# Performance work log

Measured on AMD Instinct MI355X. Metric: run time of the kernel, lower is better.

The kernel has to match this reference:

```python
import jax, jax.numpy as jnp
import numpy as np
from jax import lax

SL, BS, D, H, T = 256, 64, 1024, 512, 17
BN_EPS = 1e-5


def setup_inputs() -> dict:
    key = jax.random.key(0)
    ks = jax.random.split(key, 16)
    k = 1.0 / np.sqrt(H)
    u = lambda kk, shape: jax.random.uniform(kk, shape, jnp.float32, -k, k)
    word_input = jax.random.normal(ks[0], (SL, BS, D), jnp.float32)
    lengths = jax.random.randint(ks[1], (BS,), SL // 2, SL + 1)
    mask = jnp.arange(SL)[:, None] < lengths[None, :]  # (SL, BS), first step all valid
    labels = jax.random.randint(ks[2], (SL, BS), 0, T)
    return dict(
        word_input=word_input, mask=mask, labels=labels,
        w_ih_f=u(ks[3], (4 * H, D)), w_hh_f=u(ks[4], (4 * H, H)),
        b_ih_f=u(ks[5], (4 * H,)), b_hh_f=u(ks[6], (4 * H,)),
        w_ih_b=u(ks[7], (4 * H, D)), w_hh_b=u(ks[8], (4 * H, H)),
        b_ih_b=u(ks[9], (4 * H,)), b_hh_b=u(ks[10], (4 * H,)),
        bn_gamma=jnp.ones((2 * H,), jnp.float32), bn_beta=jnp.zeros((2 * H,), jnp.float32),
        lin_w=u(ks[11], (T, 2 * H)), lin_b=u(ks[12], (T,)),
        crf_start=0.1 * jax.random.normal(ks[13], (T,), jnp.float32),
        crf_end=0.1 * jax.random.normal(ks[14], (T,), jnp.float32),
        crf_trans=0.1 * jax.random.normal(ks[15], (T, T), jnp.float32),
    )


def _lstm_dir(x, w_ih, w_hh, b_ih, b_hh, reverse):
    # x: (SL, BS, D); PyTorch gate order i, f, g, o
    B = x.shape[1]
    h0 = jnp.zeros((B, H), x.dtype)
    xg = jnp.einsum('sbd,gd->sbg', x, w_ih) + b_ih + b_hh  # precompute input projections

    def step(carry, xt):
        h, c = carry
        g = xt + h @ w_hh.T
        i, f, gg, o = jnp.split(g, 4, axis=-1)
        c = jax.nn.sigmoid(f) * c + jax.nn.sigmoid(i) * jnp.tanh(gg)
        h = jax.nn.sigmoid(o) * jnp.tanh(c)
        return (h, c), h

    _, hs = lax.scan(step, (h0, h0), xg, reverse=reverse)
    return hs  # (SL, BS, H)


def _crf_llh(E, y, m, start, end, trans):
    # E: (B, L, T) batch-first emissions; y: (B, L) int; m: (B, L) bool
    B = E.shape[0]
    mf = m.astype(E.dtype)
    b = jnp.arange(B)
    # numerator (gold path score)
    emit = jnp.take_along_axis(E, y[:, :, None], axis=2)[:, :, 0]  # (B, L)
    num = start[y[:, 0]] + emit[:, 0]
    tr = trans[y[:, :-1], y[:, 1:]]  # (B, L-1)
    num = num + jnp.sum(mf[:, 1:] * (tr + emit[:, 1:]), axis=1)
    last = jnp.sum(m.astype(jnp.int32), axis=1) - 1
    num = num + end[y[b, last]]
    # partition function via forward algorithm
    alpha0 = start + E[:, 0]  # (B, T)

    def step(alpha, inp):
        e_t, m_t = inp
        nxt = jax.nn.logsumexp(alpha[:, :, None] + trans[None], axis=1) + e_t
        return jnp.where(m_t[:, None], nxt, alpha), None

    alpha, _ = lax.scan(step, alpha0, (E[:, 1:].transpose(1, 0, 2), m[:, 1:].T))
    Z = jax.nn.logsumexp(alpha + end, axis=1)
    return jnp.sum(num - Z)


def _viterbi(E, m, start, end, trans):
    # E: (B, L, T); m: (B, L) bool -> padded tags (B, L)
    B = E.shape[0]
    b = jnp.arange(B)
    score0 = start + E[:, 0]  # (B, T)

    def fwd(score, inp):
        e_t, m_t = inp
        cand = score[:, :, None] + trans[None]  # (B, T, T)
        best_prev = jnp.argmax(cand, axis=1)  # (B, T)
        best = jnp.max(cand, axis=1) + e_t
        return jnp.where(m_t[:, None], best, score), best_prev

    final, history = lax.scan(fwd, score0, (E[:, 1:].transpose(1, 0, 2), m[:, 1:].T))
    last_tag = jnp.argmax(final + end, axis=1)  # (B,)

    def bwd(tag, inp):
        bp, m_t = inp
        prev = jnp.where(m_t, bp[b, tag], tag)
        return prev, tag

    tag0, tags_rest = lax.scan(bwd, last_tag, (history, m[:, 1:].T), reverse=True)
    tags = jnp.concatenate([tag0[None], tags_rest], axis=0).T  # (B, L)
    return jnp.where(m, tags, 0)


def _forward(word_input, mask, labels, w_ih_f, w_hh_f, b_ih_f, b_hh_f,
             w_ih_b, w_hh_b, b_ih_b, b_hh_b, bn_gamma, bn_beta, lin_w, lin_b,
             crf_start, crf_end, crf_trans):
    hf = _lstm_dir(word_input, w_ih_f, w_hh_f, b_ih_f, b_hh_f, reverse=False)
    hb = _lstm_dir(word_input, w_ih_b, w_hh_b, b_ih_b, b_hh_b, reverse=True)
    lstm_out = jnp.concatenate([hf, hb], axis=-1)  # (SL, BS, 2H)
    x = lstm_out.reshape(-1, 2 * H)
    mean = x.mean(0)
    var = x.var(0)  # biased, as in torch BN training normalization
    xn = (x - mean) / jnp.sqrt(var + BN_EPS) * bn_gamma + bn_beta
    logits = xn @ lin_w.T + lin_b  # (SL*BS, T)
    E = logits.reshape(SL, BS, T).transpose(1, 0, 2)  # batch-first (B, L, T)
    m = mask.T  # (B, L)
    loss = -_crf_llh(E, labels.T, m, crf_start, crf_end, crf_trans)
    preds = _viterbi(E, m, crf_start, crf_end, crf_trans)
    return loss, preds


def reference(word_input, mask, labels, w_ih_f, w_hh_f, b_ih_f, b_hh_f,
              w_ih_b, w_hh_b, b_ih_b, b_hh_b, bn_gamma, bn_beta, lin_w, lin_b,
              crf_start, crf_end, crf_trans):
    return _forward(word_input, mask, labels, w_ih_f, w_hh_f, b_ih_f, b_hh_f,
                    w_ih_b, w_hh_b, b_ih_b, b_hh_b, bn_gamma, bn_beta, lin_w, lin_b,
                    crf_start, crf_end, crf_trans)
```

## Files before the change

### kernel.cpp

```cpp
#include <hip/hip_runtime.h>
#include <hip/hip_bf16.h>
#include <math.h>

#define SL 256
#define BS 64
#define DI 1024
#define HH 512
#define TT 17
#define NR (SL*BS)
#define G4 (4*HH)
#define C2 (2*HH)
#define NBLK 128

__device__ __forceinline__ float sigm(float x) { return 1.f / (1.f + expf(-x)); }

typedef float vfloat4 __attribute__((ext_vector_type(4)));

__device__ __forceinline__ void coh_load4(float4& d, const float* p) {
    asm volatile("global_load_dwordx4 %0, %1, off sc0 sc1" : "=v"(d) : "v"(p) : "memory");
}
__device__ __forceinline__ void coh_load4i(int4& d, const int* p) {
    asm volatile("global_load_dwordx4 %0, %1, off sc0 sc1" : "=v"(d) : "v"(p) : "memory");
}
__device__ __forceinline__ void coh_store4(const float4& d, float* p) {
    vfloat4 t; t.x = d.x; t.y = d.y; t.z = d.z; t.w = d.w;
    asm volatile("global_store_dwordx4 %0, %1, off sc0 sc1" :: "v"(p), "v"(t) : "memory");
}
__device__ __forceinline__ void wait_vm0() { asm volatile("s_waitcnt vmcnt(0)" ::: "memory"); }

__global__ __launch_bounds__(256) void pack_whh_v3(const float* __restrict__ whh,
                                                   float* __restrict__ wp)
{
    const int s = blockIdx.x;
    for (int idx = threadIdx.x; idx < 512 * 24; idx += 256) {
        const int k = idx / 24, c = idx % 24;
        float v = 0.f;
        if (c < 16) {
            const int g = c >> 2, uu = c & 3;
            v = whh[(size_t)(g * 512 + 4 * s + uu) * HH + k];
        }
        wp[(size_t)s * 12288 + idx] = v;
    }
}

__global__ __launch_bounds__(512) void init_flags(int* __restrict__ f)
{
    f[blockIdx.x * 512 + threadIdx.x] = 0;
}

__global__ __launch_bounds__(256) void gemm_xg(
    const float* __restrict__ A,
    const float* __restrict__ W,
    const float* __restrict__ b1,
    const float* __restrict__ b2,
    float* __restrict__ C)
{
    __shared__ float As[16][128];
    __shared__ float Bs[16][128];
    const int tid = threadIdx.x;
    const int m0 = blockIdx.x * 128;
    const int n0 = blockIdx.y * 128;
    const int tm = tid >> 4;
    const int tn = tid & 15;
    const int lr = tid >> 2;
    const int lc = (tid & 3) * 4;

    float acc[8][8];
    #pragma unroll
    for (int i = 0; i < 8; i++)
        #pragma unroll
        for (int j = 0; j < 8; j++) acc[i][j] = 0.f;

    for (int kt = 0; kt < DI; kt += 16) {
        #pragma unroll
        for (int p = 0; p < 2; p++) {
            float4 v = *(const float4*)(A + (size_t)(m0 + p * 64 + lr) * DI + kt + lc);
            As[lc + 0][p * 64 + lr] = v.x;
            As[lc + 1][p * 64 + lr] = v.y;
            As[lc + 2][p * 64 + lr] = v.z;
            As[lc + 3][p * 64 + lr] = v.w;
            float4 w = *(const float4*)(W + (size_t)(n0 + p * 64 + lr) * DI + kt + lc);
            Bs[lc + 0][p * 64 + lr] = w.x;
            Bs[lc + 1][p * 64 + lr] = w.y;
            Bs[lc + 2][p * 64 + lr] = w.z;
            Bs[lc + 3][p * 64 + lr] = w.w;
        }
        __syncthreads();
        #pragma unroll
        for (int kk = 0; kk < 16; kk++) {
            float4 a0 = *(const float4*)&As[kk][tm * 8];
            float4 a1 = *(const float4*)&As[kk][tm * 8 + 4];
            float4 bv0 = *(const float4*)&Bs[kk][tn * 8];
            float4 bv1 = *(const float4*)&Bs[kk][tn * 8 + 4];
            float a[8] = {a0.x, a0.y, a0.z, a0.w, a1.x, a1.y, a1.z, a1.w};
            float b[8] = {bv0.x, bv0.y, bv0.z, bv0.w, bv1.x, bv1.y, bv1.z, bv1.w};
            #pragma unroll
            for (int i = 0; i < 8; i++)
                #pragma unroll
                for (int j = 0; j < 8; j++)
                    acc[i][j] = fmaf(a[i], b[j], acc[i][j]);
        }
        __syncthreads();
    }
    const int g  = n0 >> 9;
    const int u0 = (n0 & 511) + tn * 8;
    const int s0 = u0 >> 2;
    #pragma unroll
    for (int i = 0; i < 8; i++) {
        const int m = m0 + tm * 8 + i;
        const int mt = m >> 6, mb = m & 63;
        #pragma unroll
        for (int sj = 0; sj < 4; sj++) {
            const int n = n0 + tn * 8 + sj * 2;
            float2 v;
            v.x = acc[i][sj * 2 + 0] + b1[n + 0] + b2[n + 0];
            v.y = acc[i][sj * 2 + 1] + b1[n + 1] + b2[n + 1];
            *(float2*)(C + ((((size_t)(s0 + (sj >> 1)) * SL + mt) * BS + mb) << 4)
                         + g * 4 + 2 * (sj & 1)) = v;
        }
    }
}

__global__ __launch_bounds__(512, 2) void lstm_flag(
    const float* __restrict__ xg_f, const float* __restrict__ xg_b,
    const float* __restrict__ wp_f, const float* __restrict__ wp_b,
    float* __restrict__ Hf, float* __restrict__ Hb,
    int* __restrict__ flag_f, int* __restrict__ flag_b,
    float* __restrict__ out,
    int dir_base)
{
    __shared__ float w_s[512 * 24];
    __shared__ float hs[128 * 68];
    __shared__ float g_s[16 * 65];
    __shared__ float hpub[256];
    float* const part = hs;

    const int dir = dir_base + (blockIdx.x >> 7);
    const int s   = blockIdx.x & 127;
    const float* xg  = dir ? xg_b : xg_f;
    const float* wp  = dir ? wp_b : wp_f;
    float* Hbuf      = dir ? Hb : Hf;
    int*   flag      = dir ? flag_b : flag_f;
    const int reverse = dir;
    const int col_off = dir * HH;

    const int tid = threadIdx.x;
    const int ks  = tid >> 4;
    const int bt  = (tid >> 1) & 7;
    const int ct  = tid & 1;
    const int wv  = tid >> 6;

    {
        const float4* src = (const float4*)(wp + (size_t)s * 12288);
        float4* dst = (float4*)w_s;
        for (int i = tid; i < 3072; i += 512) dst[i] = src[i];
    }

    const float* xgs = xg + (size_t)s * (SL * 1024);
    float cst = 0.f;
    float4 r[4];
    float4 acc[8][2];

    for (int step = 0; step < SL; ++step) {
        const int t = reverse ? (SL - 1 - step) : step;
        const float myxg0 = xgs[t * 1024 + tid];
        const float myxg1 = xgs[t * 1024 + 512 + tid];

        if (step > 0) {
            if (tid < 32) {
                const int* fp = flag + (step - 1) * NBLK + tid * 4;
                int4 f;
                for (;;) {
                    coh_load4i(f, fp);
                    wait_vm0();
                    if (f.x & f.y & f.z & f.w) break;
                    __builtin_amdgcn_s_sleep(1);
                }
            }
            __syncthreads();

            const float* hsrc = Hbuf + ((step + 1) & 1) * (512 * 64);
            #pragma unroll
            for (int i = 0; i < 4; ++i)
                coh_load4(r[i], hsrc + (size_t)(i * 512 + tid) * 4);

            #pragma unroll
            for (int i = 0; i < 8; ++i) {
                acc[i][0] = make_float4(0.f, 0.f, 0.f, 0.f);
                acc[i][1] = make_float4(0.f, 0.f, 0.f, 0.f);
            }

            for (int kc = 0; kc < 4; ++kc) {
                if (kc) __syncthreads();
                wait_vm0();
                #pragma unroll
                for (int i = 0; i < 4; ++i) {
                    const int idx = i * 512 + tid;
                    const int k = idx >> 4, b4 = (idx & 15) * 4;
                    *(float4*)&hs[k * 68 + b4] = r[i];
                }
                __syncthreads();
                if (kc < 3) {
                    const float* base = hsrc + (size_t)(kc + 1) * 8192;
                    #pragma unroll
                    for (int i = 0; i < 4; ++i)
                        coh_load4(r[i], base + (size_t)(i * 512 + tid) * 4);
                }
                #pragma unroll
                for (int j = 0; j < 4; ++j) {
                    const int kk = ks + 32 * j;
                    const int kg = kc * 128 + kk;
                    const float4 w0 = *(const float4*)&w_s[kg * 24 + ct * 8];
                    const float4 w1 = *(const float4*)&w_s[kg * 24 + ct * 8 + 4];
                    const float* hp = &hs[kk * 68 + 8 * bt];
                    const float2 h01 = *(const float2*)(hp + 0);
                    const float2 h23 = *(const float2*)(hp + 2);
                    const float2 h45 = *(const float2*)(hp + 4);
                    const float2 h67 = *(const float2*)(hp + 6);
                    const float hv[8] = {h01.x, h01.y, h23.x, h23.y, h45.x, h45.y, h67.x, h67.y};
                    #pragma unroll
                    for (int i = 0; i < 8; ++i) {
                        acc[i][0].x = fmaf(hv[i], w0.x, acc[i][0].x);
                        acc[i][0].y = fmaf(hv[i], w0.y, acc[i][0].y);
                        acc[i][0].z = fmaf(hv[i], w0.z, acc[i][0].z);
                        acc[i][0].w = fmaf(hv[i], w0.w, acc[i][0].w);
                        acc[i][1].x = fmaf(hv[i], w1.x, acc[i][1].x);
                        acc[i][1].y = fmaf(hv[i], w1.y, acc[i][1].y);
                        acc[i][1].z = fmaf(hv[i], w1.z, acc[i][1].z);
                        acc[i][1].w = fmaf(hv[i], w1.w, acc[i][1].w);
                    }
                }
            }
            #pragma unroll
            for (int i = 0; i < 8; ++i)
                #pragma unroll
                for (int p = 0; p < 2; ++p) {
                    acc[i][p].x += __shfl_xor(acc[i][p].x, 16);
                    acc[i][p].y += __shfl_xor(acc[i][p].y, 16);
                    acc[i][p].z += __shfl_xor(acc[i][p].z, 16);
                    acc[i][p].w += __shfl_xor(acc[i][p].w, 16);
                    acc[i][p].x += __shfl_xor(acc[i][p].x, 32);
                    acc[i][p].y += __shfl_xor(acc[i][p].y, 32);
                    acc[i][p].z += __shfl_xor(acc[i][p].z, 32);
                    acc[i][p].w += __shfl_xor(acc[i][p].w, 32);
                }
            __syncthreads();
            if ((tid & 63) < 16) {
                #pragma unroll
                for (int i = 0; i < 8; ++i) {
                    const int base = wv * 1088 + (8 * bt + i) * 16 + ct * 8 + bt * 8;
                    *(float4*)&part[base + 0] = acc[i][0];
                    *(float4*)&part[base + 4] = acc[i][1];
                }
            }
            __syncthreads();
        }

        {
            float v0 = myxg0, v1 = myxg1;
            if (step > 0) {
                const int gA = tid, gB = tid + 512;
                const int iA = gA + 8 * (gA >> 7);
                const int iB = gB + 8 * (gB >> 7);
                #pragma unroll
                for (int w = 0; w < 8; ++w) {
                    v0 += part[w * 1088 + iA];
                    v1 += part[w * 1088 + iB];
                }
            }
            g_s[(tid & 15) * 65 + (tid >> 4)] = v0;
            {
                const int gB = tid + 512;
                g_s[(gB & 15) * 65 + (gB >> 4)] = v1;
            }
        }
        __syncthreads();

        if (tid < 256) {
            const int b = tid & 63, uu = tid >> 6;
            const float ig = sigm(g_s[(0  + uu) * 65 + b]);
            const float fg = sigm(g_s[(4  + uu) * 65 + b]);
            const float gg = tanhf(g_s[(8  + uu) * 65 + b]);
            const float og = sigm(g_s[(12 + uu) * 65 + b]);
            cst = fg * cst + ig * gg;
            hpub[tid] = og * tanhf(cst);
        }
        __syncthreads();
        if (tid < 16) {
            const float4 v = *(const float4*)&hpub[tid * 16];
            coh_store4(v, Hbuf + (step & 1) * (512 * 64) + s * 256 + tid * 16);
            *(float4*)(out + (size_t)(col_off + 4 * s + (tid >> 2)) * NR
                           + (size_t)t * 64 + (tid & 3) * 16) = v;
        }
        if (wv == 0) wait_vm0();
        __syncthreads();
        if (tid == 0)
            __hip_atomic_store(flag + step * NBLK + s, 1,
                               __ATOMIC_RELEASE, __HIP_MEMORY_SCOPE_AGENT);
    }
}

__global__ __launch_bounds__(256) void bn_stats(
    const float* __restrict__ X2, float* __restrict__ mean, float* __restrict__ istd)
{
    const int ch = blockIdx.x, tid = threadIdx.x;
    const float* base = X2 + (size_t)ch * NR;
    __shared__ float red[256];
    float s = 0.f;
    for (int i = tid * 4; i < NR; i += 1024) {
        const float4 v = *(const float4*)(base + i);
        s += v.x + v.y + v.z + v.w;
    }
    red[tid] = s; __syncthreads();
    for (int o = 128; o; o >>= 1) { if (tid < o) red[tid] += red[tid + o]; __syncthreads(); }
    const float mu = red[0] * (1.f / NR);
    __syncthreads();
    float vv = 0.f;
    for (int i = tid * 4; i < NR; i += 1024) {
        const float4 v = *(const float4*)(base + i);
        const float d0 = v.x - mu, d1 = v.y - mu, d2 = v.z - mu, d3 = v.w - mu;
        vv += d0 * d0 + d1 * d1 + d2 * d2 + d3 * d3;
    }
    red[tid] = vv; __syncthreads();
    for (int o = 128; o; o >>= 1) { if (tid < o) red[tid] += red[tid + o]; __syncthreads(); }
    if (tid == 0) { mean[ch] = mu; istd[ch] = rsqrtf(red[0] * (1.f / NR) + 1e-5f); }
}

__global__ void fold_lin(const float* __restrict__ lin_w, const float* __restrict__ lin_b,
                         const float* __restrict__ gamma, const float* __restrict__ beta,
                         const float* __restrict__ mean, const float* __restrict__ istd,
                         float* __restrict__ Wf, float* __restrict__ ct)
{
    const int t = blockIdx.x, tid = threadIdx.x;
    __shared__ float red[256];
    float acc = 0.f;
    for (int cc = tid; cc < C2; cc += 256) {
        const float w = lin_w[t * C2 + cc];
        const float g = gamma[cc] * istd[cc];
        Wf[t * C2 + cc] = w * g;
        acc = fmaf(beta[cc] - mean[cc] * g, w, acc);
    }
    red[tid] = acc; __syncthreads();
    for (int o = 128; o; o >>= 1) { if (tid < o) red[tid] += red[tid + o]; __syncthreads(); }
    if (tid == 0) ct[t] = red[0] + lin_b[t];
}

__global__ __launch_bounds__(256) void emit_logits(
    const float* __restrict__ X2, const float* __restrict__ Wf,
    const float* __restrict__ ct, float* __restrict__ E)
{
    __shared__ float ps[256 * TT];
    const int t = blockIdx.x;
    const int tid = threadIdx.x;
    const int b = tid & 63, p = tid >> 6;
    const float* xb = X2 + (size_t)t * 64 + b;

    float acc[TT];
    #pragma unroll
    for (int k = 0; k < TT; k++) acc[k] = 0.f;

    for (int c0 = p * 256; c0 < p * 256 + 256; c0 += 4) {
        const float x0 = xb[(size_t)(c0 + 0) * NR];
        const float x1 = xb[(size_t)(c0 + 1) * NR];
        const float x2 = xb[(size_t)(c0 + 2) * NR];
        const float x3 = xb[(size_t)(c0 + 3) * NR];
        #pragma unroll
        for (int k = 0; k < TT; k++) {
            const float4 w = *(const float4*)&Wf[k * C2 + c0];
            acc[k] = fmaf(x0, w.x, fmaf(x1, w.y, fmaf(x2, w.z, fmaf(x3, w.w, acc[k]))));
        }
    }
    #pragma unroll
    for (int k = 0; k < TT; k++) ps[tid * TT + k] = acc[k];
    __syncthreads();
    if (tid < 64) {
        float* Er = E + ((size_t)tid * SL + t) * TT;
        #pragma unroll
        for (int k = 0; k < TT; k++) {
            float v = ct[k];
            #pragma unroll
            for (int q = 0; q < 4; q++) v += ps[(q * 64 + tid) * TT + k];
            Er[k] = v;
        }
    }
}

__global__ __launch_bounds__(64) void crf_llh(
    const float* __restrict__ E, const int* __restrict__ mask,
    const int* __restrict__ labels, const float* __restrict__ startv,
    const float* __restrict__ endv, const float* __restrict__ trans,
    float* __restrict__ res)
{
    const int b = blockIdx.x, lane = threadIdx.x;
    __shared__ float tr[TT][TT];
    for (int i = lane; i < TT * TT; i += 64) tr[i / TT][i % TT] = trans[i];
    __syncthreads();
    const float* Eb = E + (size_t)b * SL * TT;
    const int j = (lane < TT) ? lane : 0;

    float alpha = -1e30f;
    if (lane < TT) alpha = startv[lane] + Eb[lane];

    float numacc = 0.f; int len = 0;
    for (int t = lane; t < SL; t += 64) {
        const int mt = mask[t * BS + b];
        len += (mt != 0);
        if (t >= 1 && mt) {
            const int yp = labels[(t - 1) * BS + b];
            const int yt = labels[t * BS + b];
            numacc += tr[yp][yt] + Eb[t * TT + yt];
        }
    }
    for (int off = 32; off; off >>= 1) {
        numacc += __shfl_xor(numacc, off);
        len += __shfl_xor(len, off);
    }

    for (int t = 1; t < SL; ++t) {
        const int mt = mask[t * BS + b];
        if (mt) {
            float av[TT];
            #pragma unroll
            for (int i = 0; i < TT; i++) av[i] = __shfl(alpha, i);
            const float e = (lane < TT) ? Eb[t * TT + lane] : 0.f;
            float mx = -1e30f;
            #pragma unroll
            for (int i = 0; i < TT; i++) mx = fmaxf(mx, av[i] + tr[i][j]);
            float ssum = 0.f;
            #pragma unroll
            for (int i = 0; i < TT; i++) ssum += expf(av[i] + tr[i][j] - mx);
            const float nxt = mx + logf(ssum) + e;
            if (lane < TT) alpha = nxt;
        }
    }
    float v = (lane < TT) ? alpha + endv[lane] : -1e30f;
    float mx = v;
    for (int off = 32; off; off >>= 1) mx = fmaxf(mx, __shfl_xor(mx, off));
    float se = (lane < TT) ? expf(v - mx) : 0.f;
    for (int off = 32; off; off >>= 1) se += __shfl_xor(se, off);
    const float Z = mx + logf(se);

    if (lane == 0) {
        const int y0 = labels[b];
        float num = startv[y0] + Eb[y0] + numacc;
        const int last = len - 1;
        const int yl = labels[last * BS + b];
        num += endv[yl];
        res[b] = num - Z;
    }
}

__global__ __launch_bounds__(64) void loss_reduce(const float* __restrict__ res, float* __restrict__ out)
{
    const int lane = threadIdx.x;
    float v = res[lane];
    for (int off = 32; off; off >>= 1) v += __shfl_xor(v, off);
    if (lane == 0) out[0] = -v;
}

__global__ __launch_bounds__(64) void viterbi(
    const float* __restrict__ E, const int* __restrict__ mask,
    const float* __restrict__ startv, const float* __restrict__ endv,
    const float* __restrict__ trans, float* __restrict__ preds)
{
    const int b = blockIdx.x, lane = threadIdx.x;
    __shared__ float tr[TT][TT];
    __shared__ unsigned char bp[SL][TT];
    for (int i = lane; i < TT * TT; i += 64) tr[i / TT][i % TT] = trans[i];
    __syncthreads();
    const float* Eb = E + (size_t)b * SL * TT;
    const int j = (lane < TT) ? lane : 0;

    float score = (lane < TT) ? startv[lane] + Eb[lane] : -1e30f;
    for (int t = 1; t < SL; ++t) {
        float av[TT];
        #pragma unroll
        for (int i = 0; i < TT; i++) av[i] = __shfl(score, i);
        float best = -1e30f; int bi = 0;
        #pragma unroll
        for (int i = 0; i < TT; i++) {
            const float cand = av[i] + tr[i][j];
            if (cand > best) { best = cand; bi = i; }
        }
        const int mt = mask[t * BS + b];
        if (lane < TT) {
            bp[t][lane] = (unsigned char)bi;
            if (mt) score = best + Eb[t * TT + lane];
        }
    }
    float v = (lane < TT) ? score + endv[lane] : -1e30f;
    float mx = v;
    for (int off = 32; off; off >>= 1) mx = fmaxf(mx, __shfl_xor(mx, off));
    unsigned long long ball = __ballot(v == mx);
    const int last_tag = __ffsll(ball) - 1;
    __syncthreads();

    if (lane == 0) {
        int tag = last_tag;
        float* pb = preds + (size_t)b * SL;
        for (int t = SL - 1; t >= 1; --t) {
            const int mt = mask[t * BS + b];
            pb[t] = mt ? (float)tag : 0.f;
            if (mt) tag = bp[t][tag];
        }
        pb[0] = mask[b] ? (float)tag : 0.f;
    }
}

extern "C" void kernel_launch(void* const* d_in, const int* in_sizes, int n_in,
                              void* d_out, int out_size, void* d_ws, size_t ws_size,
                              hipStream_t stream)
{
    const float* word    = (const float*)d_in[0];
    const int*   mask    = (const int*)  d_in[1];
    const int*   labels  = (const int*)  d_in[2];
    const float* w_ih_f  = (const float*)d_in[3];
    const float* w_hh_f  = (const float*)d_in[4];
    const float* b_ih_f  = (const float*)d_in[5];
    const float* b_hh_f  = (const float*)d_in[6];
    const float* w_ih_b  = (const float*)d_in[7];
    const float* w_hh_b  = (const float*)d_in[8];
    const float* b_ih_b  = (const float*)d_in[9];
    const float* b_hh_b  = (const float*)d_in[10];
    const float* gamma   = (const float*)d_in[11];
    const float* beta    = (const float*)d_in[12];
    const float* lin_w   = (const float*)d_in[13];
    const float* lin_b   = (const float*)d_in[14];
    const float* c_start = (const float*)d_in[15];
    const float* c_end   = (const float*)d_in[16];
    const float* c_trans = (const float*)d_in[17];
    float* out = (float*)d_out;
    (void)in_sizes; (void)n_in; (void)out_size;

    char* ws = (char*)d_ws;
    size_t off = 0;
    auto alloc = [&](size_t bytes) {
        void* p = ws + off;
        off += (bytes + 255) & ~(size_t)255;
        return p;
    };
    float* XG_F  = (float*)alloc((size_t)NR * G4 * 4);
    float* WPK_F = (float*)alloc((size_t)128 * 12288 * 4);
    float* WPK_B = (float*)alloc((size_t)128 * 12288 * 4);
    float* LOUT  = (float*)alloc((size_t)NR * C2 * 4);
    float* HB_F  = (float*)alloc((size_t)2 * 512 * 64 * 4);
    float* HB_B  = (float*)alloc((size_t)2 * 512 * 64 * 4);
    int*   FLAGS = (int*)  alloc((size_t)2 * SL * NBLK * 4);
    float* MEAN  = (float*)alloc(C2 * 4);
    float* ISTD  = (float*)alloc(C2 * 4);
    float* WF    = (float*)alloc(TT * C2 * 4);
    float* CT    = (float*)alloc(TT * 4);
    float* Ebuf  = (float*)alloc((size_t)BS * SL * TT * 4);
    float* RES   = (float*)alloc(BS * 4);
    float* XG_B  = (float*)alloc((size_t)NR * G4 * 4);
    const bool merged = (ws_size >= off);
    if (!merged) XG_B = XG_F;

    init_flags<<<128, 512, 0, stream>>>(FLAGS);
    pack_whh_v3<<<128, 256, 0, stream>>>(w_hh_f, WPK_F);
    pack_whh_v3<<<128, 256, 0, stream>>>(w_hh_b, WPK_B);

    if (merged) {
        gemm_xg<<<dim3(NR / 128, G4 / 128), 256, 0, stream>>>(word, w_ih_f, b_ih_f, b_hh_f, XG_F);
        gemm_xg<<<dim3(NR / 128, G4 / 128), 256, 0, stream>>>(word, w_ih_b, b_ih_b, b_hh_b, XG_B);
        lstm_flag<<<2 * NBLK, 512, 0, stream>>>(XG_F, XG_B, WPK_F, WPK_B, HB_F, HB_B,
                                                FLAGS, FLAGS + SL * NBLK, LOUT, 0);
    } else {
        gemm_xg<<<dim3(NR / 128, G4 / 128), 256, 0, stream>>>(word, w_ih_f, b_ih_f, b_hh_f, XG_F);
        lstm_flag<<<NBLK, 512, 0, stream>>>(XG_F, XG_B, WPK_F, WPK_B, HB_F, HB_B,
                                            FLAGS, FLAGS + SL * NBLK, LOUT, 0);
        gemm_xg<<<dim3(NR / 128, G4 / 128), 256, 0, stream>>>(word, w_ih_b, b_ih_b, b_hh_b, XG_F);
        lstm_flag<<<NBLK, 512, 0, stream>>>(XG_F, XG_B, WPK_F, WPK_B, HB_F, HB_B,
                                            FLAGS, FLAGS + SL * NBLK, LOUT, 1);
    }

    bn_stats<<<C2, 256, 0, stream>>>(LOUT, MEAN, ISTD);
    fold_lin<<<TT, 256, 0, stream>>>(lin_w, lin_b, gamma, beta, MEAN, ISTD, WF, CT);
    emit_logits<<<SL, 256, 0, stream>>>(LOUT, WF, CT, Ebuf);

    crf_llh<<<BS, 64, 0, stream>>>(Ebuf, mask, labels, c_start, c_end, c_trans, RES);
    loss_reduce<<<1, 64, 0, stream>>>(RES, out);
    viterbi<<<BS, 64, 0, stream>>>(Ebuf, mask, c_start, c_end, c_trans, out + 1);
}
```

Baseline: 9.514 ms.

## Double-buffer xg GEMM tiles and halve LSTM hidden-state staging rounds

The input-projection GEMM now double-buffers its shared-memory A/B tiles and prefetches the next k-slice into registers while computing the current one, which removes one barrier per iteration. In the recurrent LSTM kernel, the hidden state is staged in two chunks of 256 rows instead of four chunks of 128. This halves the barriers and load-wait rounds per timestep. The cost is more shared memory (the LSTM hs buffer doubles) and more registers, which can reduce occupancy under launch_bounds(512,2).

```diff
diff --git a/kernel.cpp b/kernel.cpp
--- a/kernel.cpp
+++ b/kernel.cpp
@@ -55,8 +55,8 @@
     const float* __restrict__ b2,
     float* __restrict__ C)
 {
-    __shared__ float As[16][128];
-    __shared__ float Bs[16][128];
+    __shared__ float As[2][16][128];
+    __shared__ float Bs[2][16][128];
     const int tid = threadIdx.x;
     const int m0 = blockIdx.x * 128;
     const int n0 = blockIdx.y * 128;
@@ -71,27 +71,33 @@
         #pragma unroll
         for (int j = 0; j < 8; j++) acc[i][j] = 0.f;
 
-    for (int kt = 0; kt < DI; kt += 16) {
-        #pragma unroll
-        for (int p = 0; p < 2; p++) {
-            float4 v = *(const float4*)(A + (size_t)(m0 + p * 64 + lr) * DI + kt + lc);
-            As[lc + 0][p * 64 + lr] = v.x;
-            As[lc + 1][p * 64 + lr] = v.y;
-            As[lc + 2][p * 64 + lr] = v.z;
-            As[lc + 3][p * 64 + lr] = v.w;
-            float4 w = *(const float4*)(W + (size_t)(n0 + p * 64 + lr) * DI + kt + lc);
-            Bs[lc + 0][p * 64 + lr] = w.x;
-            Bs[lc + 1][p * 64 + lr] = w.y;
-            Bs[lc + 2][p * 64 + lr] = w.z;
-            Bs[lc + 3][p * 64 + lr] = w.w;
-        }
-        __syncthreads();
+    float4 ra[2], rb[2];
+    #pragma unroll
+    for (int p = 0; p < 2; p++) {
+        ra[p] = *(const float4*)(A + (size_t)(m0 + p * 64 + lr) * DI + lc);
+        rb[p] = *(const float4*)(W + (size_t)(n0 + p * 64 + lr) * DI + lc);
+    }
+    int cur = 0;
+    #pragma unroll
+    for (int p = 0; p < 2; p++) {
+        As[cur][lc + 0][p * 64 + lr] = ra[p].x;
+        As[cur][lc + 1][p * 64 + lr] = ra[p].y;
+        As[cur][lc + 2][p * 64 + lr] = ra[p].z;
+        As[cur][lc + 3][p * 64 + lr] = ra[p].w;
+        Bs[cur][lc + 0][p * 64 + lr] = rb[p].x;
+        Bs[cur][lc + 1][p * 64 + lr] = rb[p].y;
+        Bs[cur][lc + 2][p * 64 + lr] = rb[p].z;
+        Bs[cur][lc + 3][p * 64 + lr] = rb[p].w;
+    }
+    __syncthreads();
+
+    auto compute = [&](int buf) {
         #pragma unroll
         for (int kk = 0; kk < 16; kk++) {
-            float4 a0 = *(const float4*)&As[kk][tm * 8];
-            float4 a1 = *(const float4*)&As[kk][tm * 8 + 4];
-            float4 bv0 = *(const float4*)&Bs[kk][tn * 8];
-            float4 bv1 = *(const float4*)&Bs[kk][tn * 8 + 4];
+            float4 a0  = *(const float4*)&As[buf][kk][tm * 8];
+            float4 a1  = *(const float4*)&As[buf][kk][tm * 8 + 4];
+            float4 bv0 = *(const float4*)&Bs[buf][kk][tn * 8];
+            float4 bv1 = *(const float4*)&Bs[buf][kk][tn * 8 + 4];
             float a[8] = {a0.x, a0.y, a0.z, a0.w, a1.x, a1.y, a1.z, a1.w};
             float b[8] = {bv0.x, bv0.y, bv0.z, bv0.w, bv1.x, bv1.y, bv1.z, bv1.w};
             #pragma unroll
@@ -100,8 +106,31 @@
                 for (int j = 0; j < 8; j++)
                     acc[i][j] = fmaf(a[i], b[j], acc[i][j]);
         }
+    };
+
+    for (int kt = 16; kt < DI; kt += 16) {
+        #pragma unroll
+        for (int p = 0; p < 2; p++) {
+            ra[p] = *(const float4*)(A + (size_t)(m0 + p * 64 + lr) * DI + kt + lc);
+            rb[p] = *(const float4*)(W + (size_t)(n0 + p * 64 + lr) * DI + kt + lc);
+        }
+        compute(cur);
+        #pragma unroll
+        for (int p = 0; p < 2; p++) {
+            As[cur ^ 1][lc + 0][p * 64 + lr] = ra[p].x;
+            As[cur ^ 1][lc + 1][p * 64 + lr] = ra[p].y;
+            As[cur ^ 1][lc + 2][p * 64 + lr] = ra[p].z;
+            As[cur ^ 1][lc + 3][p * 64 + lr] = ra[p].w;
+            Bs[cur ^ 1][lc + 0][p * 64 + lr] = rb[p].x;
+            Bs[cur ^ 1][lc + 1][p * 64 + lr] = rb[p].y;
+            Bs[cur ^ 1][lc + 2][p * 64 + lr] = rb[p].z;
+            Bs[cur ^ 1][lc + 3][p * 64 + lr] = rb[p].w;
+        }
         __syncthreads();
-    }
+        cur ^= 1;
+    }
+    compute(cur);
+
     const int g  = n0 >> 9;
     const int u0 = (n0 & 511) + tn * 8;
     const int s0 = u0 >> 2;
@@ -130,7 +159,7 @@
     int dir_base)
 {
     __shared__ float w_s[512 * 24];
-    __shared__ float hs[128 * 68];
+    __shared__ float hs[256 * 68];
     __shared__ float g_s[16 * 65];
     __shared__ float hpub[256];
     float* const part = hs;
@@ -158,7 +187,7 @@
 
     const float* xgs = xg + (size_t)s * (SL * 1024);
     float cst = 0.f;
-    float4 r[4];
+    float4 r[8];
     float4 acc[8][2];
 
     for (int step = 0; step < SL; ++step) {
@@ -181,7 +210,7 @@
 
             const float* hsrc = Hbuf + ((step + 1) & 1) * (512 * 64);
             #pragma unroll
-            for (int i = 0; i < 4; ++i)
+            for (int i = 0; i < 8; ++i)
                 coh_load4(r[i], hsrc + (size_t)(i * 512 + tid) * 4);
 
             #pragma unroll
@@ -190,46 +219,47 @@
                 acc[i][1] = make_float4(0.f, 0.f, 0.f, 0.f);
             }
 
-            for (int kc = 0; kc < 4; ++kc) {
-                if (kc) __syncthreads();
+            #pragma unroll
+            for (int sc = 0; sc < 2; ++sc) {
+                if (sc) __syncthreads();
                 wait_vm0();
                 #pragma unroll
-                for (int i = 0; i < 4; ++i) {
+                for (int i = 0; i < 8; ++i) {
                     const int idx = i * 512 + tid;
-                    const int k = idx >> 4, b4 = (idx & 15) * 4;
-                    *(float4*)&hs[k * 68 + b4] = r[i];
+                    *(float4*)&hs[(idx >> 4) * 68 + (idx & 15) * 4] = r[i];
                 }
                 __syncthreads();
-                if (kc < 3) {
-                    const float* base = hsrc + (size_t)(kc + 1) * 8192;
+                if (sc == 0) {
                     #pragma unroll
-                    for (int i = 0; i < 4; ++i)
-                        coh_load4(r[i], base + (size_t)(i * 512 + tid) * 4);
+                    for (int i = 0; i < 8; ++i)
+                        coh_load4(r[i], hsrc + (size_t)(4096 + i * 512 + tid) * 4);
                 }
                 #pragma unroll
-                for (int j = 0; j < 4; ++j) {
-                    const int kk = ks + 32 * j;
-                    const int kg = kc * 128 + kk;
-                    const float4 w0 = *(const float4*)&w_s[kg * 24 + ct * 8];
-                    const float4 w1 = *(const float4*)&w_s[kg * 24 + ct * 8 + 4];
-                    const float* hp = &hs[kk * 68 + 8 * bt];
-                    const float2 h01 = *(const float2*)(hp + 0);
-                    const float2 h23 = *(const float2*)(hp + 2);
-                    const float2 h45 = *(const float2*)(hp + 4);
-                    const float2 h67 = *(const float2*)(hp + 6);
-                    const float hv[8] = {h01.x, h01.y, h23.x, h23.y, h45.x, h45.y, h67.x, h67.y};
+                for (int half = 0; half < 2; ++half)
                     #pragma unroll
-                    for (int i = 0; i < 8; ++i) {
-                        acc[i][0].x = fmaf(hv[i], w0.x, acc[i][0].x);
-                        acc[i][0].y = fmaf(hv[i], w0.y, acc[i][0].y);
-                        acc[i][0].z = fmaf(hv[i], w0.z, acc[i][0].z);
-                        acc[i][0].w = fmaf(hv[i], w0.w, acc[i][0].w);
-                        acc[i][1].x = fmaf(hv[i], w1.x, acc[i][1].x);
-                        acc[i][1].y = fmaf(hv[i], w1.y, acc[i][1].y);
-                        acc[i][1].z = fmaf(hv[i], w1.z, acc[i][1].z);
-                        acc[i][1].w = fmaf(hv[i], w1.w, acc[i][1].w);
+                    for (int j = 0; j < 4; ++j) {
+                        const int kl = half * 128 + ks + 32 * j;
+                        const int kg = sc * 256 + kl;
+                        const float4 w0 = *(const float4*)&w_s[kg * 24 + ct * 8];
+                        const float4 w1 = *(const float4*)&w_s[kg * 24 + ct * 8 + 4];
+                        const float* hp = &hs[kl * 68 + 8 * bt];
+                        const float2 h01 = *(const float2*)(hp + 0);
+                        const float2 h23 = *(const float2*)(hp + 2);
+                        const float2 h45 = *(const float2*)(hp + 4);
+                        const float2 h67 = *(const float2*)(hp + 6);
+                        const float hv[8] = {h01.x, h01.y, h23.x, h23.y, h45.x, h45.y, h67.x, h67.y};
+                        #pragma unroll
+                        for (int i = 0; i < 8; ++i) {
+                            acc[i][0].x = fmaf(hv[i], w0.x, acc[i][0].x);
+                            acc[i][0].y = fmaf(hv[i], w0.y, acc[i][0].y);
+                            acc[i][0].z = fmaf(hv[i], w0.z, acc[i][0].z);
+                            acc[i][0].w = fmaf(hv[i], w0.w, acc[i][0].w);
+                            acc[i][1].x = fmaf(hv[i], w1.x, acc[i][1].x);
+                            acc[i][1].y = fmaf(hv[i], w1.y, acc[i][1].y);
+                            acc[i][1].z = fmaf(hv[i], w1.z, acc[i][1].z);
+                            acc[i][1].w = fmaf(hv[i], w1.w, acc[i][1].w);
+                        }
                     }
-                }
             }
             #pragma unroll
             for (int i = 0; i < 8; ++i)
```

Result: slower. 10.15 ms (+6.7%).

## Use split-bf16 MFMA for the input projection GEMM

Applied to the files above, without the earlier changes.

Replaces the FP32 SIMT shared-memory GEMM for the input-gate projections with a matrix-core kernel. Each FP32 operand is split into high and low bf16 parts, and three bf16 MFMA products (hi*hi, hi*lo, lo*hi) approximate FP32 accuracy. Operands are loaded straight from global memory into registers with no LDS staging, which may cost memory efficiency. Accuracy is slightly lower than true FP32, and the output stores are now scalar and scattered.

```diff
diff --git a/kernel.cpp b/kernel.cpp
--- a/kernel.cpp
+++ b/kernel.cpp
@@ -15,6 +15,8 @@
 __device__ __forceinline__ float sigm(float x) { return 1.f / (1.f + expf(-x)); }
 
 typedef float vfloat4 __attribute__((ext_vector_type(4)));
+typedef __attribute__((ext_vector_type(8))) short short8v;
+typedef __attribute__((ext_vector_type(4))) float f32x4;
 
 __device__ __forceinline__ void coh_load4(float4& d, const float* p) {
     asm volatile("global_load_dwordx4 %0, %1, off sc0 sc1" : "=v"(d) : "v"(p) : "memory");
@@ -27,6 +29,95 @@
     asm volatile("global_store_dwordx4 %0, %1, off sc0 sc1" :: "v"(p), "v"(t) : "memory");
 }
 __device__ __forceinline__ void wait_vm0() { asm volatile("s_waitcnt vmcnt(0)" ::: "memory"); }
+
+__device__ __forceinline__ void split8(const float4& x0, const float4& x1,
+                                       short8v& h, short8v& l)
+{
+    const float xs[8] = {x0.x, x0.y, x0.z, x0.w, x1.x, x1.y, x1.z, x1.w};
+    #pragma unroll
+    for (int j = 0; j < 8; ++j) {
+        const uint u   = __float_as_uint(xs[j]);
+        const float hf = __uint_as_float(u & 0xFFFF0000u);
+        h[j] = (short)(u >> 16);
+        const float lo = xs[j] - hf;
+        const uint v   = __float_as_uint(lo);
+        l[j] = (short)((v + 0x7FFFu + ((v >> 16) & 1u)) >> 16);
+    }
+}
+
+__global__ __launch_bounds__(256) void gemm_xg_mfma(
+    const float* __restrict__ A,
+    const float* __restrict__ W,
+    const float* __restrict__ b1,
+    const float* __restrict__ b2,
+    float* __restrict__ C)
+{
+    const int tid  = threadIdx.x;
+    const int lane = tid & 63;
+    const int w    = tid >> 6;
+    const int wm   = w >> 1, wn = w & 1;
+    const int m0   = blockIdx.x * 128 + wm * 64;
+    const int n0   = blockIdx.y * 128 + wn * 64;
+    const int lr   = lane & 15;
+    const int lk   = (lane >> 4) * 8;
+
+    const float* pA = A + (size_t)(m0 + lr) * DI + lk;
+    const float* pB = W + (size_t)(n0 + lr) * DI + lk;
+
+    f32x4 acc[4][4];
+    #pragma unroll
+    for (int i = 0; i < 4; i++)
+        #pragma unroll
+        for (int j = 0; j < 4; j++) {
+            acc[i][j][0] = 0.f; acc[i][j][1] = 0.f;
+            acc[i][j][2] = 0.f; acc[i][j][3] = 0.f;
+        }
+
+    for (int k0 = 0; k0 < DI; k0 += 32) {
+        short8v ah[4], al[4], bh[4], bl[4];
+        #pragma unroll
+        for (int i = 0; i < 4; i++) {
+            const float4 a0 = *(const float4*)(pA + (size_t)i * 16 * DI + k0);
+            const float4 a1 = *(const float4*)(pA + (size_t)i * 16 * DI + k0 + 4);
+            split8(a0, a1, ah[i], al[i]);
+            const float4 b0 = *(const float4*)(pB + (size_t)i * 16 * DI + k0);
+            const float4 b1v = *(const float4*)(pB + (size_t)i * 16 * DI + k0 + 4);
+            split8(b0, b1v, bh[i], bl[i]);
+        }
+        #pragma unroll
+        for (int i = 0; i < 4; i++)
+            #pragma unroll
+            for (int j = 0; j < 4; j++)
+                acc[i][j] = __builtin_amdgcn_mfma_f32_16x16x32_bf16(ah[i], bh[j], acc[i][j], 0, 0, 0);
+        #pragma unroll
+        for (int i = 0; i < 4; i++)
+            #pragma unroll
+            for (int j = 0; j < 4; j++)
+                acc[i][j] = __builtin_amdgcn_mfma_f32_16x16x32_bf16(ah[i], bl[j], acc[i][j], 0, 0, 0);
+        #pragma unroll
+        for (int i = 0; i < 4; i++)
+            #pragma unroll
+            for (int j = 0; j < 4; j++)
+                acc[i][j] = __builtin_amdgcn_mfma_f32_16x16x32_bf16(al[i], bh[j], acc[i][j], 0, 0, 0);
+    }
+
+    #pragma unroll
+    for (int j = 0; j < 4; j++) {
+        const int n  = n0 + j * 16 + lr;
+        const float bs = b1[n] + b2[n];
+        const int u  = n & 511, g = n >> 9;
+        const int s0 = u >> 2,  c = g * 4 + (u & 3);
+        #pragma unroll
+        for (int i = 0; i < 4; i++) {
+            #pragma unroll
+            for (int r = 0; r < 4; r++) {
+                const int m  = m0 + i * 16 + (lane >> 4) * 4 + r;
+                const int mt = m >> 6, mb = m & 63;
+                C[((((size_t)s0 * SL + mt) * BS + mb) << 4) + c] = acc[i][j][r] + bs;
+            }
+        }
+    }
+}
 
 __global__ __launch_bounds__(256) void pack_whh_v3(const float* __restrict__ whh,
                                                    float* __restrict__ wp)
@@ -46,79 +137,6 @@
 __global__ __launch_bounds__(512) void init_flags(int* __restrict__ f)
 {
     f[blockIdx.x * 512 + threadIdx.x] = 0;
-}
-
-__global__ __launch_bounds__(256) void gemm_xg(
-    const float* __restrict__ A,
-    const float* __restrict__ W,
-    const float* __restrict__ b1,
-    const float* __restrict__ b2,
-    float* __restrict__ C)
-{
-    __shared__ float As[16][128];
-    __shared__ float Bs[16][128];
-    const int tid = threadIdx.x;
-    const int m0 = blockIdx.x * 128;
-    const int n0 = blockIdx.y * 128;
-    const int tm = tid >> 4;
-    const int tn = tid & 15;
-    const int lr = tid >> 2;
-    const int lc = (tid & 3) * 4;
-
-    float acc[8][8];
-    #pragma unroll
-    for (int i = 0; i < 8; i++)
-        #pragma unroll
-        for (int j = 0; j < 8; j++) acc[i][j] = 0.f;
-
-    for (int kt = 0; kt < DI; kt += 16) {
-        #pragma unroll
-        for (int p = 0; p < 2; p++) {
-            float4 v = *(const float4*)(A + (size_t)(m0 + p * 64 + lr) * DI + kt + lc);
-            As[lc + 0][p * 64 + lr] = v.x;
-            As[lc + 1][p * 64 + lr] = v.y;
-            As[lc + 2][p * 64 + lr] = v.z;
-            As[lc + 3][p * 64 + lr] = v.w;
-            float4 w = *(const float4*)(W + (size_t)(n0 + p * 64 + lr) * DI + kt + lc);
-            Bs[lc + 0][p * 64 + lr] = w.x;
-            Bs[lc + 1][p * 64 + lr] = w.y;
-            Bs[lc + 2][p * 64 + lr] = w.z;
-            Bs[lc + 3][p * 64 + lr] = w.w;
-        }
-        __syncthreads();
-        #pragma unroll
-        for (int kk = 0; kk < 16; kk++) {
-            float4 a0 = *(const float4*)&As[kk][tm * 8];
-            float4 a1 = *(const float4*)&As[kk][tm * 8 + 4];
-            float4 bv0 = *(const float4*)&Bs[kk][tn * 8];
-            float4 bv1 = *(const float4*)&Bs[kk][tn * 8 + 4];
-            float a[8] = {a0.x, a0.y, a0.z, a0.w, a1.x, a1.y, a1.z, a1.w};
-            float b[8] = {bv0.x, bv0.y, bv0.z, bv0.w, bv1.x, bv1.y, bv1.z, bv1.w};
-            #pragma unroll
-            for (int i = 0; i < 8; i++)
-                #pragma unroll
-                for (int j = 0; j < 8; j++)
-                    acc[i][j] = fmaf(a[i], b[j], acc[i][j]);
-        }
-        __syncthreads();
-    }
-    const int g  = n0 >> 9;
-    const int u0 = (n0 & 511) + tn * 8;
-    const int s0 = u0 >> 2;
-    #pragma unroll
-    for (int i = 0; i < 8; i++) {
-        const int m = m0 + tm * 8 + i;
-        const int mt = m >> 6, mb = m & 63;
-        #pragma unroll
-        for (int sj = 0; sj < 4; sj++) {
-            const int n = n0 + tn * 8 + sj * 2;
-            float2 v;
-            v.x = acc[i][sj * 2 + 0] + b1[n + 0] + b2[n + 0];
-            v.y = acc[i][sj * 2 + 1] + b1[n + 1] + b2[n + 1];
-            *(float2*)(C + ((((size_t)(s0 + (sj >> 1)) * SL + mt) * BS + mb) << 4)
-                         + g * 4 + 2 * (sj & 1)) = v;
-        }
-    }
 }
 
 __global__ __launch_bounds__(512, 2) void lstm_flag(
@@ -561,15 +579,15 @@
     pack_whh_v3<<<128, 256, 0, stream>>>(w_hh_b, WPK_B);
 
     if (merged) {
-        gemm_xg<<<dim3(NR / 128, G4 / 128), 256, 0, stream>>>(word, w_ih_f, b_ih_f, b_hh_f, XG_F);
-        gemm_xg<<<dim3(NR / 128, G4 / 128), 256, 0, stream>>>(word, w_ih_b, b_ih_b, b_hh_b, XG_B);
+        gemm_xg_mfma<<<dim3(NR / 128, G4 / 128), 256, 0, stream>>>(word, w_ih_f, b_ih_f, b_hh_f, XG_F);
+        gemm_xg_mfma<<<dim3(NR / 128, G4 / 128), 256, 0, stream>>>(word, w_ih_b, b_ih_b, b_hh_b, XG_B);
         lstm_flag<<<2 * NBLK, 512, 0, stream>>>(XG_F, XG_B, WPK_F, WPK_B, HB_F, HB_B,
                                                 FLAGS, FLAGS + SL * NBLK, LOUT, 0);
     } else {
-        gemm_xg<<<dim3(NR / 128, G4 / 128), 256, 0, stream>>>(word, w_ih_f, b_ih_f, b_hh_f, XG_F);
+        gemm_xg_mfma<<<dim3(NR / 128, G4 / 128), 256, 0, stream>>>(word, w_ih_f, b_ih_f, b_hh_f, XG_F);
         lstm_flag<<<NBLK, 512, 0, stream>>>(XG_F, XG_B, WPK_F, WPK_B, HB_F, HB_B,
                                             FLAGS, FLAGS + SL * NBLK, LOUT, 0);
-        gemm_xg<<<dim3(NR / 128, G4 / 128), 256, 0, stream>>>(word, w_ih_b, b_ih_b, b_hh_b, XG_F);
+        gemm_xg_mfma<<<dim3(NR / 128, G4 / 128), 256, 0, stream>>>(word, w_ih_b, b_ih_b, b_hh_b, XG_F);
         lstm_flag<<<NBLK, 512, 0, stream>>>(XG_F, XG_B, WPK_F, WPK_B, HB_F, HB_B,
                                             FLAGS, FLAGS + SL * NBLK, LOUT, 1);
     }
```

Result: faster. 8.895 ms (-6.5%).
